# Performance work log

Measured on AMD Instinct MI355X. Metric: run time of the kernel, lower is better.

The kernel has to match this reference:

```python
import jax, jax.numpy as jnp
from jax import lax
import numpy as np

B, T, F, H, L, HOR = 512, 512, 16, 256, 3, 24


def setup_inputs() -> dict:
    key = jax.random.key(0)
    ks = jax.random.split(key, 9)
    s = 0.05
    x = jax.random.normal(ks[0], (B, T, F), dtype=jnp.float32)
    # PyTorch LSTM params: gate order (i, f, g, o), W_ih [4H, in], W_hh [4H, H]
    W_ih0 = jax.random.normal(ks[1], (4 * H, F), dtype=jnp.float32) * s
    W_ih12 = jax.random.normal(ks[2], (L - 1, 4 * H, H), dtype=jnp.float32) * s
    W_hh = jax.random.normal(ks[3], (L, 4 * H, H), dtype=jnp.float32) * s
    b_ih = jax.random.normal(ks[4], (L, 4 * H), dtype=jnp.float32) * s
    b_hh = jax.random.normal(ks[5], (L, 4 * H), dtype=jnp.float32) * s
    fc_W = jax.random.normal(ks[6], (HOR, H), dtype=jnp.float32) * s
    fc_b = jax.random.normal(ks[7], (HOR,), dtype=jnp.float32) * s
    return {"x": x, "W_ih0": W_ih0, "W_ih12": W_ih12, "W_hh": W_hh,
            "b_ih": b_ih, "b_hh": b_hh, "fc_W": fc_W, "fc_b": fc_b}


def _lstm_layer(x, W_ih, W_hh, b_ih, b_hh):
    # x: [B, T, in] -> h sequence [B, T, H]
    Bn = x.shape[0]
    Hn = W_hh.shape[1]
    # precompute input contribution for all timesteps (one big GEMM)
    xg = jnp.einsum('bti,gi->btg', x, W_ih) + b_ih  # [B, T, 4H]
    W_hh_T = W_hh.T  # [H, 4H]

    def step(carry, xg_t):
        h, c = carry
        gates = xg_t + h @ W_hh_T + b_hh  # [B, 4H]
        i, f, g, o = jnp.split(gates, 4, axis=-1)
        c = jax.nn.sigmoid(f) * c + jax.nn.sigmoid(i) * jnp.tanh(g)
        h = jax.nn.sigmoid(o) * jnp.tanh(c)
        return (h, c), h

    h0 = jnp.zeros((Bn, Hn), x.dtype)
    c0 = jnp.zeros((Bn, Hn), x.dtype)
    _, hs = lax.scan(step, (h0, c0), jnp.swapaxes(xg, 0, 1))  # [T, B, H]
    return jnp.swapaxes(hs, 0, 1)


def reference(x, W_ih0, W_ih12, W_hh, b_ih, b_hh, fc_W, fc_b):
    h = _lstm_layer(x, W_ih0, W_hh[0], b_ih[0], b_hh[0])
    for l in range(1, L):
        h = _lstm_layer(h, W_ih12[l - 1], W_hh[l], b_ih[l], b_hh[l])
    last_hidden = h[:, -1, :]  # [B, H]
    return last_hidden @ fc_W.T + fc_b  # [B, horizon]
```

## Files before the change

kernel.cpp:

```cpp
#include <hip/hip_runtime.h>
#include <hip/hip_bf16.h>
#include <stdint.h>

#define Bsz 512
#define Tsz 512
#define Fsz 16
#define Hsz 256
#define HORZ 24

#define NG 8
#define NBT 8
#define BT 64
#define USL 32
#define PD 4
#define HBUF_ELEMS ((size_t)3*PD*Bsz*Hsz)
#define NFLAGS (3*NG*NBT)
#define AROW_B 512
#define ABUF_B (BT*AROW_B)
#define HTILE_B (BT*64)
#define SMEM_B (3*ABUF_B + HTILE_B)

typedef float  f32x4  __attribute__((ext_vector_type(4)));
typedef float  f32x16 __attribute__((ext_vector_type(16)));
typedef __bf16 bf16x8 __attribute__((ext_vector_type(8)));
typedef uint32_t u32x2 __attribute__((ext_vector_type(2)));
typedef uint32_t u32x4 __attribute__((ext_vector_type(4)));

__device__ __forceinline__ float sigm(float v){ return 1.f/(1.f+__expf(-v)); }

__device__ __forceinline__ bf16x8 ld_sc01_b128(const void* p){
  bf16x8 r;
  asm volatile("global_load_dwordx4 %0, %1, off sc0 sc1" : "=&v"(r) : "v"(p) : "memory");
  return r;
}
__device__ __forceinline__ u32x2 ld_b64_async(const void* p){
  u32x2 r;
  asm volatile("global_load_dwordx2 %0, %1, off" : "=&v"(r) : "v"(p) : "memory");
  return r;
}
__device__ __forceinline__ void st_sc01_b64(void* p, uint64_t v){
  asm volatile("global_store_dwordx2 %0, %1, off sc0 sc1" :: "v"(p), "v"(v) : "memory");
}
__device__ __forceinline__ void st_sc01_b32(void* p, uint32_t v){
  asm volatile("global_store_dword %0, %1, off sc0 sc1" :: "v"(p), "v"(v) : "memory");
}
__device__ __forceinline__ uint32_t ld_sc01_b32(const void* p){
  uint32_t r;
  asm volatile("global_load_dword %0, %1, off sc0 sc1\n\ts_waitcnt vmcnt(0)"
    : "=&v"(r) : "v"(p) : "memory");
  return r;
}
__device__ __forceinline__ void wait_flag(const unsigned int* fp, int target){
  int guard = 0;
  while ((int)ld_sc01_b32(fp) < target){
    __builtin_amdgcn_s_sleep(1);
    if (++guard > (1<<18)) break;
  }
}

template<bool L0>
__device__ __forceinline__ void lstm_body(
    int l, int g, int nb, int tid,
    const float* __restrict__ xin,
    const float* __restrict__ Wih0,
    const float* __restrict__ Wih12,
    const float* __restrict__ Whh,
    const float* __restrict__ bih,
    const float* __restrict__ bhh,
    __bf16* __restrict__ hb,
    unsigned int* __restrict__ flags,
    char* smem)
{
  char* ain0  = smem;
  char* ain1  = smem + ABUF_B;
  char* hrc   = smem + 2*ABUF_B;
  char* htile = smem + 3*ABUF_B;

  const int lane = tid & 63;
  const int wid  = tid >> 6;
  const int wm   = wid >> 2;
  const int wn   = wid & 3;
  const int b0   = nb * BT;
  const int m0   = wm * 32;
  const int n0   = wn * 32;

  const int colL = n0 + (lane & 31);
  const int hi   = lane >> 5;
  const int kg8  = hi * 8;
  const int kg16 = hi * 16;
  const int R    = (colL&3)*Hsz + g*USL + (colL>>2);
  const float bias = bih[l*4*Hsz + R] + bhh[l*4*Hsz + R];
  const int rowA = m0 + (lane & 31);
  const int swzA = (rowA & 7) << 4;

  constexpr int NC = L0 ? 17 : 32;
  bf16x8 w[NC];
  {
    const float* recB = Whh + ((size_t)l*4*Hsz + R)*Hsz;
    #pragma unroll
    for (int c=0;c<NC;++c){
      const float* p;
      if constexpr (L0) p = (c==0) ? (Wih0 + (size_t)R*Fsz + kg8)
                                   : (recB + (c-1)*16 + kg8);
      else              p = (c<16) ? (Wih12 + ((size_t)(l-1)*4*Hsz + R)*Hsz + c*16 + kg8)
                                   : (recB + (c-16)*16 + kg8);
      f32x4 u0 = *(const f32x4*)p;
      f32x4 u1 = *(const f32x4*)(p+4);
      bf16x8 t;
      #pragma unroll
      for (int j=0;j<4;++j){ t[j]=(__bf16)u0[j]; t[j+4]=(__bf16)u1[j]; }
      w[c] = t;
    }
  }

  const int srow = tid >> 3, sq = tid & 7;
  const int sswz = (srow & 7) << 4;
  const size_t sgrow = (size_t)(b0 + srow) * Hsz;

  float cst[16];
  #pragma unroll
  for (int i=0;i<16;++i) cst[i]=0.f;

  unsigned int* myflag = flags + ((l*NG+g)*NBT + nb);
  const bool q2 = ((colL & 3) == 2);
  auto slotp = [&](int ll, int s){ return hb + ((size_t)ll*PD + (s&3))*Bsz*Hsz; };

  {
    u32x4 z = {0,0,0,0};
    #pragma unroll
    for (int j=0;j<4;++j) *(u32x4*)(hrc + tid*64 + j*16) = z;
  }
  if constexpr (L0){
    u32x2 xv = ld_b64_async(xin + ((size_t)(b0+srow)*Tsz + 0)*Fsz + sq*2);
    asm volatile("s_waitcnt vmcnt(0)" ::: "memory");
    __builtin_amdgcn_sched_barrier(0);
    char* d = ain0 + srow*32 + sq*4;
    *(__bf16*)(d)   = (__bf16)__uint_as_float(xv[0]);
    *(__bf16*)(d+2) = (__bf16)__uint_as_float(xv[1]);
  } else {
    if (tid < 8) wait_flag(flags + (((l-1)*NG + tid)*NBT + nb), 1);
    __syncthreads();
    const __bf16* src = slotp(l-1,0) + sgrow + sq*32;
    bf16x8 av[4];
    #pragma unroll
    for (int j=0;j<4;++j) av[j] = ld_sc01_b128(src + j*8);
    asm volatile("s_waitcnt vmcnt(0)" ::: "memory");
    __builtin_amdgcn_sched_barrier(0);
    #pragma unroll
    for (int j=0;j<4;++j)
      *(bf16x8*)(ain0 + srow*AROW_B + ((sq*64 + j*16) ^ sswz)) = av[j];
  }
  __syncthreads();

  for (int t=0; t<Tsz; ++t){
    {
      const unsigned int* fp=nullptr; int target=0;
      int grp = tid>>3, gg = tid&7;
      if      (grp==0 && !L0 && t+1<Tsz) { fp = flags + (((l-1)*NG+gg)*NBT+nb); target=t+2; }
      else if (grp==1 && t>0)            { fp = flags + ((l*NG+gg)*NBT+nb);     target=t;   }
      else if (grp==2 && l<2 && t>=PD)   { fp = flags + (((l+1)*NG+gg)*NBT+nb); target=t-(PD-1); }
      if (fp) wait_flag(fp, target);
      __syncthreads();
    }

    char* aprd = (t&1) ? ain1 : ain0;
    char* apwr = (t&1) ? ain0 : ain1;
    bf16x8 hiv[4];
    const bool pfon = (!L0) && (t+1 < Tsz);

    if constexpr (L0){
      u32x2 xv = ld_b64_async(xin + ((size_t)(b0+srow)*Tsz + t)*Fsz + sq*2);
      bf16x8 hrv[4];
      if (t > 0){
        const __bf16* src = slotp(l,t-1) + sgrow + sq*32;
        #pragma unroll
        for (int j=0;j<4;++j) hrv[j] = ld_sc01_b128(src + j*8);
      }
      asm volatile("s_waitcnt vmcnt(0)" ::: "memory");
      __builtin_amdgcn_sched_barrier(0);
      char* d = ain0 + srow*32 + sq*4;
      *(__bf16*)(d)   = (__bf16)__uint_as_float(xv[0]);
      *(__bf16*)(d+2) = (__bf16)__uint_as_float(xv[1]);
      if (t > 0){
        #pragma unroll
        for (int j=0;j<4;++j)
          *(bf16x8*)(hrc + srow*AROW_B + ((sq*64 + j*16) ^ sswz)) = hrv[j];
      }
      __syncthreads();
    } else {
      if (t > 0){
        bf16x8 hrv[4];
        const __bf16* src = slotp(l,t-1) + sgrow + sq*32;
        #pragma unroll
        for (int j=0;j<4;++j) hrv[j] = ld_sc01_b128(src + j*8);
        asm volatile("s_waitcnt vmcnt(0)" ::: "memory");
        __builtin_amdgcn_sched_barrier(0);
        #pragma unroll
        for (int j=0;j<4;++j)
          *(bf16x8*)(hrc + srow*AROW_B + ((sq*64 + j*16) ^ sswz)) = hrv[j];
      }
      if (pfon){
        const __bf16* s2 = slotp(l-1,t+1) + sgrow + sq*32;
        #pragma unroll
        for (int j=0;j<4;++j) hiv[j] = ld_sc01_b128(s2 + j*8);
      }
      __syncthreads();
    }

    f32x16 acc;
    #pragma unroll
    for (int i=0;i<16;++i) acc[i]=0.f;
    #pragma unroll
    for (int c=0;c<NC;++c){
      bf16x8 af;
      if constexpr (L0){
        if (c==0) af = *(const bf16x8*)(ain0 + rowA*32 + kg16);
        else      af = *(const bf16x8*)(hrc + rowA*AROW_B + ((((c-1)*32) + kg16) ^ swzA));
      } else {
        if (c<16) af = *(const bf16x8*)(aprd + rowA*AROW_B + (((c*32) + kg16) ^ swzA));
        else      af = *(const bf16x8*)(hrc  + rowA*AROW_B + ((((c-16)*32) + kg16) ^ swzA));
      }
      acc = __builtin_amdgcn_mfma_f32_32x32x16_bf16(af, w[c], acc, 0,0,0);
    }

    #pragma unroll
    for (int i=0;i<16;++i){
      float v  = acc[i] + bias;
      float vv = q2 ? 2.f*v : v;
      float sg = sigm(vv);
      float act = q2 ? (2.f*sg - 1.f) : sg;
      float a1 = __shfl_xor(act,1,64);
      float a2 = __shfl_xor(act,2,64);
      float a3 = __shfl_xor(act,3,64);
      if ((lane&3)==0){
        float cn = a1*cst[i] + act*a2;
        cst[i] = cn;
        float th = 2.f*sigm(2.f*cn) - 1.f;
        float hv = a3*th;
        int r = (i&3) + 8*(i>>2) + 4*hi;
        int unit = colL >> 2;
        *(__bf16*)(htile + (m0 + r)*64 + unit*2) = (__bf16)hv;
      }
    }
    __syncthreads();

    {
      uint64_t v = *(const uint64_t*)(htile + srow*64 + sq*8);
      st_sc01_b64(slotp(l,t) + sgrow + g*USL + sq*4, v);
    }
    asm volatile("s_waitcnt vmcnt(0)" ::: "memory");
    __builtin_amdgcn_sched_barrier(0);
    if (pfon){
      #pragma unroll
      for (int j=0;j<4;++j)
        *(bf16x8*)(apwr + srow*AROW_B + ((sq*64 + j*16) ^ sswz)) = hiv[j];
    }
    __syncthreads();
    if (tid==0) st_sc01_b32(myflag, (uint32_t)(t+1));
  }
}

__global__ __launch_bounds__(512, 2) void lstm_persist(
    const float* __restrict__ xin,
    const float* __restrict__ Wih0,
    const float* __restrict__ Wih12,
    const float* __restrict__ Whh,
    const float* __restrict__ bih,
    const float* __restrict__ bhh,
    __bf16* __restrict__ hb,
    unsigned int* __restrict__ flags)
{
  __shared__ __align__(16) char smem[SMEM_B];
  const int bid = blockIdx.x;
  const int l   = bid >> 6;
  const int g   = (bid >> 3) & 7;
  const int nb  = bid & 7;
  const int tid = threadIdx.x;
  if (l == 0)
    lstm_body<true >(l,g,nb,tid, xin,Wih0,Wih12,Whh,bih,bhh, hb,flags, smem);
  else
    lstm_body<false>(l,g,nb,tid, xin,Wih0,Wih12,Whh,bih,bhh, hb,flags, smem);
}

__global__ void fc_kernel(const __bf16* __restrict__ hb,
                          const float* __restrict__ fcW,
                          const float* __restrict__ fcb,
                          float* __restrict__ out)
{
  __shared__ float hs[Hsz];
  int b = blockIdx.x;
  const __bf16* hp = hb + ((size_t)(2*PD + ((Tsz-1)&(PD-1))))*Bsz*Hsz + (size_t)b*Hsz;
  for (int i = threadIdx.x; i < Hsz; i += 64) hs[i] = (float)hp[i];
  __syncthreads();
  int o = threadIdx.x;
  if (o < HORZ) {
    float a = fcb[o];
    #pragma unroll 8
    for (int u=0; u<Hsz; ++u) a += hs[u]*fcW[o*Hsz + u];
    out[b*HORZ + o] = a;
  }
}

extern "C" void kernel_launch(void* const* d_in, const int* in_sizes, int n_in,
                              void* d_out, int out_size, void* d_ws, size_t ws_size,
                              hipStream_t stream)
{
  const float* x     = (const float*)d_in[0];
  const float* Wih0  = (const float*)d_in[1];
  const float* Wih12 = (const float*)d_in[2];
  const float* Whh   = (const float*)d_in[3];
  const float* bih   = (const float*)d_in[4];
  const float* bhh   = (const float*)d_in[5];
  const float* fcW   = (const float*)d_in[6];
  const float* fcb   = (const float*)d_in[7];

  __bf16* hb = (__bf16*)d_ws;
  unsigned int* flags = (unsigned int*)((char*)d_ws + HBUF_ELEMS*2);
  size_t clr = HBUF_ELEMS*2 + (size_t)NFLAGS*4;
  hipMemsetAsync(d_ws, 0, clr, stream);

  hipLaunchKernelGGL(lstm_persist, dim3(3*NG*NBT), dim3(512), 0, stream,
                     x, Wih0, Wih12, Whh, bih, bhh, hb, flags);
  hipLaunchKernelGGL(fc_kernel, dim3(Bsz), dim3(64), 0, stream, hb, fcW, fcb, (float*)d_out);
}
```

Baseline: 3.918 ms.

## Replace per-step flag polling with poison-sentinel data polling in ring buffer

Removes most per-timestep flag waits and instead has consumers poll the hidden-state slots directly until no NaN sentinel (poison) values remain. Producers write poison two slots ahead to invalidate stale data, and the ring depth grows from 4 to 8. A flag-based backpressure wait on the downstream layer now runs only every fourth step. The workspace is initialised with a custom poison-fill kernel instead of a memset. This cuts flag round-trips and barriers on the serial critical path, but relies on the sentinel never appearing as a real value and on 64-bit store atomicity, and it adds an extra store per step.

```diff
diff --git a/kernel.cpp b/kernel.cpp
--- a/kernel.cpp
+++ b/kernel.cpp
@@ -12,7 +12,7 @@
 #define NBT 8
 #define BT 64
 #define USL 32
-#define PD 4
+#define PD 8
 #define HBUF_ELEMS ((size_t)3*PD*Bsz*Hsz)
 #define NFLAGS (3*NG*NBT)
 #define AROW_B 512
@@ -20,6 +20,9 @@
 #define HTILE_B (BT*64)
 #define SMEM_B (3*ABUF_B + HTILE_B)
 
+#define POISON   0x7FC07FC0u
+#define POISON64 0x7FC07FC07FC07FC0ull
+
 typedef float  f32x4  __attribute__((ext_vector_type(4)));
 typedef float  f32x16 __attribute__((ext_vector_type(16)));
 typedef __bf16 bf16x8 __attribute__((ext_vector_type(8)));
@@ -55,6 +58,27 @@
   while ((int)ld_sc01_b32(fp) < target){
     __builtin_amdgcn_s_sleep(1);
     if (++guard > (1<<18)) break;
+  }
+}
+__device__ __forceinline__ bool poison_free(const bf16x8* v){
+  bool ok = true;
+  #pragma unroll
+  for (int j=0;j<4;++j){
+    u32x4 uv = __builtin_bit_cast(u32x4, v[j]);
+    ok = ok && (uv[0] != POISON) && (uv[2] != POISON);
+  }
+  return ok;
+}
+__device__ __forceinline__ void poll_load4(bf16x8* dst, const __bf16* src){
+  int guard = 0;
+  for(;;){
+    #pragma unroll
+    for (int j=0;j<4;++j) dst[j] = ld_sc01_b128(src + j*8);
+    asm volatile("s_waitcnt vmcnt(0)" ::: "memory");
+    __builtin_amdgcn_sched_barrier(0);
+    if (poison_free(dst)) break;
+    __builtin_amdgcn_s_sleep(4);
+    if (++guard > (1<<16)) break;
   }
 }
 
@@ -123,7 +147,7 @@
 
   unsigned int* myflag = flags + ((l*NG+g)*NBT + nb);
   const bool q2 = ((colL & 3) == 2);
-  auto slotp = [&](int ll, int s){ return hb + ((size_t)ll*PD + (s&3))*Bsz*Hsz; };
+  auto slotp = [&](int ll, int s){ return hb + ((size_t)ll*PD + (s&(PD-1)))*Bsz*Hsz; };
 
   {
     u32x4 z = {0,0,0,0};
@@ -138,14 +162,8 @@
     *(__bf16*)(d)   = (__bf16)__uint_as_float(xv[0]);
     *(__bf16*)(d+2) = (__bf16)__uint_as_float(xv[1]);
   } else {
-    if (tid < 8) wait_flag(flags + (((l-1)*NG + tid)*NBT + nb), 1);
-    __syncthreads();
-    const __bf16* src = slotp(l-1,0) + sgrow + sq*32;
     bf16x8 av[4];
-    #pragma unroll
-    for (int j=0;j<4;++j) av[j] = ld_sc01_b128(src + j*8);
-    asm volatile("s_waitcnt vmcnt(0)" ::: "memory");
-    __builtin_amdgcn_sched_barrier(0);
+    poll_load4(av, slotp(l-1,0) + sgrow + sq*32);
     #pragma unroll
     for (int j=0;j<4;++j)
       *(bf16x8*)(ain0 + srow*AROW_B + ((sq*64 + j*16) ^ sswz)) = av[j];
@@ -153,31 +171,24 @@
   __syncthreads();
 
   for (int t=0; t<Tsz; ++t){
-    {
-      const unsigned int* fp=nullptr; int target=0;
-      int grp = tid>>3, gg = tid&7;
-      if      (grp==0 && !L0 && t+1<Tsz) { fp = flags + (((l-1)*NG+gg)*NBT+nb); target=t+2; }
-      else if (grp==1 && t>0)            { fp = flags + ((l*NG+gg)*NBT+nb);     target=t;   }
-      else if (grp==2 && l<2 && t>=PD)   { fp = flags + (((l+1)*NG+gg)*NBT+nb); target=t-(PD-1); }
-      if (fp) wait_flag(fp, target);
+    if (l < 2 && (t & 3) == 0){
+      if (tid < 8 && t >= 4)
+        wait_flag(flags + (((l+1)*NG + tid)*NBT + nb), t-3);
       __syncthreads();
     }
 
     char* aprd = (t&1) ? ain1 : ain0;
     char* apwr = (t&1) ? ain0 : ain1;
     bf16x8 hiv[4];
+    const __bf16* pfsrc = nullptr;
     const bool pfon = (!L0) && (t+1 < Tsz);
 
     if constexpr (L0){
       u32x2 xv = ld_b64_async(xin + ((size_t)(b0+srow)*Tsz + t)*Fsz + sq*2);
       bf16x8 hrv[4];
-      if (t > 0){
-        const __bf16* src = slotp(l,t-1) + sgrow + sq*32;
-        #pragma unroll
-        for (int j=0;j<4;++j) hrv[j] = ld_sc01_b128(src + j*8);
-      }
-      asm volatile("s_waitcnt vmcnt(0)" ::: "memory");
-      __builtin_amdgcn_sched_barrier(0);
+      if (t > 0) poll_load4(hrv, slotp(l,t-1) + sgrow + sq*32);
+      else { asm volatile("s_waitcnt vmcnt(0)" ::: "memory");
+             __builtin_amdgcn_sched_barrier(0); }
       char* d = ain0 + srow*32 + sq*4;
       *(__bf16*)(d)   = (__bf16)__uint_as_float(xv[0]);
       *(__bf16*)(d+2) = (__bf16)__uint_as_float(xv[1]);
@@ -190,19 +201,15 @@
     } else {
       if (t > 0){
         bf16x8 hrv[4];
-        const __bf16* src = slotp(l,t-1) + sgrow + sq*32;
-        #pragma unroll
-        for (int j=0;j<4;++j) hrv[j] = ld_sc01_b128(src + j*8);
-        asm volatile("s_waitcnt vmcnt(0)" ::: "memory");
-        __builtin_amdgcn_sched_barrier(0);
+        poll_load4(hrv, slotp(l,t-1) + sgrow + sq*32);
         #pragma unroll
         for (int j=0;j<4;++j)
           *(bf16x8*)(hrc + srow*AROW_B + ((sq*64 + j*16) ^ sswz)) = hrv[j];
       }
       if (pfon){
-        const __bf16* s2 = slotp(l-1,t+1) + sgrow + sq*32;
+        pfsrc = slotp(l-1,t+1) + sgrow + sq*32;
         #pragma unroll
-        for (int j=0;j<4;++j) hiv[j] = ld_sc01_b128(s2 + j*8);
+        for (int j=0;j<4;++j) hiv[j] = ld_sc01_b128(pfsrc + j*8);
       }
       __syncthreads();
     }
@@ -246,11 +253,13 @@
 
     {
       uint64_t v = *(const uint64_t*)(htile + srow*64 + sq*8);
-      st_sc01_b64(slotp(l,t) + sgrow + g*USL + sq*4, v);
+      st_sc01_b64(slotp(l,t)   + sgrow + g*USL + sq*4, v);
+      st_sc01_b64(slotp(l,t+2) + sgrow + g*USL + sq*4, POISON64);
     }
     asm volatile("s_waitcnt vmcnt(0)" ::: "memory");
     __builtin_amdgcn_sched_barrier(0);
     if (pfon){
+      if (!poison_free(hiv)) poll_load4(hiv, pfsrc);
       #pragma unroll
       for (int j=0;j<4;++j)
         *(bf16x8*)(apwr + srow*AROW_B + ((sq*64 + j*16) ^ sswz)) = hiv[j];
@@ -280,6 +289,17 @@
     lstm_body<true >(l,g,nb,tid, xin,Wih0,Wih12,Whh,bih,bhh, hb,flags, smem);
   else
     lstm_body<false>(l,g,nb,tid, xin,Wih0,Wih12,Whh,bih,bhh, hb,flags, smem);
+}
+
+__global__ void init_ws(uint32_t* __restrict__ hb32, uint32_t* __restrict__ flags)
+{
+  size_t i = (size_t)blockIdx.x*blockDim.x + threadIdx.x;
+  size_t n = (HBUF_ELEMS*2)/16;
+  if (i < n){
+    u32x4 v = {POISON, POISON, POISON, POISON};
+    *(u32x4*)(hb32 + i*4) = v;
+  }
+  if (i < NFLAGS) flags[i] = 0;
 }
 
 __global__ void fc_kernel(const __bf16* __restrict__ hb,
@@ -316,8 +336,10 @@
 
   __bf16* hb = (__bf16*)d_ws;
   unsigned int* flags = (unsigned int*)((char*)d_ws + HBUF_ELEMS*2);
-  size_t clr = HBUF_ELEMS*2 + (size_t)NFLAGS*4;
-  hipMemsetAsync(d_ws, 0, clr, stream);
+
+  size_t nchunk = (HBUF_ELEMS*2)/16;
+  int ib = (int)((nchunk + 255) / 256);
+  hipLaunchKernelGGL(init_ws, dim3(ib), dim3(256), 0, stream, (uint32_t*)hb, flags);
 
   hipLaunchKernelGGL(lstm_persist, dim3(3*NG*NBT), dim3(512), 0, stream,
                      x, Wih0, Wih12, Whh, bih, bhh, hb, flags);
```

New measurement: 3.195 ms. 1.23x faster.
